# Kernel tuning notes

Hardware: AMD Instinct MI355X
Metric: run time of the kernel (lower is better)

Reference implementation:

```python
import jax, jax.numpy as jnp
import numpy as np

N_PER_GRAPH = 28
E_PER_GRAPH = 56
B = 16384
C = 128
LN_EPS = 1e-5


def setup_inputs() -> dict:
    key = jax.random.key(0)
    k0, k1, k2 = jax.random.split(key, 3)
    N = B * N_PER_GRAPH
    x = jax.random.normal(k0, (N, C), dtype=jnp.float32)
    # graph-local random edges, offset per graph so edge_weights.repeat(B) lines up
    local = jax.random.randint(k1, (2, B * E_PER_GRAPH), 0, N_PER_GRAPH)
    offset = jnp.repeat(jnp.arange(B, dtype=jnp.int64) * N_PER_GRAPH, E_PER_GRAPH)
    edge_index = (local.astype(jnp.int64) + offset[None, :])
    W = jax.random.normal(k2, (C, C), dtype=jnp.float32) * (1.0 / np.sqrt(C))
    bias = jnp.zeros((C,), jnp.float32)
    edge_weights = jnp.ones((E_PER_GRAPH,), jnp.float32)
    gamma = jnp.ones((C,), jnp.float32)
    beta = jnp.zeros((C,), jnp.float32)
    return {"x": x, "edge_index": edge_index, "W": W, "bias": bias,
            "edge_weights": edge_weights, "gamma": gamma, "beta": beta}


def _gcn_conv(x, edge_index, edge_weight, W, bias):
    # PyG GCNConv: linear -> add self loops (w=1) -> sym-normalize -> scatter-add -> +bias
    N = x.shape[0]
    src, dst = edge_index[0], edge_index[1]
    loop = jnp.arange(N, dtype=edge_index.dtype)
    src_f = jnp.concatenate([src, loop])
    dst_f = jnp.concatenate([dst, loop])
    ew_f = jnp.concatenate([edge_weight, jnp.ones((N,), x.dtype)])
    deg = jax.ops.segment_sum(ew_f, dst_f, num_segments=N)
    dinv = jnp.where(deg > 0, jax.lax.rsqrt(deg), 0.0)
    norm = dinv[src_f] * ew_f * dinv[dst_f]          # [E+N]
    h = x @ W                                        # [N, C]
    msg = h[src_f] * norm[:, None]                   # gather + scale
    agg = jax.ops.segment_sum(msg, dst_f, num_segments=N)  # scatter-add
    return agg + bias


def reference(x, edge_index, W, bias, edge_weights, gamma, beta):
    res = x  # in_channels == out_channels -> residual is Identity
    batch_size = x.shape[0] // N_PER_GRAPH
    edge_weight = jnp.tile(edge_weights, batch_size)  # == edge_weights.repeat(B)
    h = _gcn_conv(x, edge_index, edge_weight, W, bias)
    y = h + res
    mu = jnp.mean(y, axis=-1, keepdims=True)
    var = jnp.mean(jnp.square(y - mu), axis=-1, keepdims=True)
    ln = (y - mu) * jax.lax.rsqrt(var + LN_EPS) * gamma + beta
    return jax.nn.relu(ln)
```

## Files before the change

kernel.cpp:

```cpp
#include <hip/hip_runtime.h>

#define NPG 28
#define EPG 56
#define ROWS 56
#define EDG 112
#define CH 128
#define LDW 136

typedef float f32x4 __attribute__((ext_vector_type(4)));
typedef __bf16 bf16x8 __attribute__((ext_vector_type(8)));
typedef unsigned short u16;
typedef u16 u16x8 __attribute__((ext_vector_type(8)));
typedef u16 u16x4 __attribute__((ext_vector_type(4)));

__device__ __forceinline__ u16 f2bf(float f){
  union { float f; unsigned u; } v; v.f = f;
  unsigned r = (v.u + 0x7fffu + ((v.u >> 16) & 1u)) >> 16;
  return (u16)r;
}
__device__ __forceinline__ float bf2f(u16 h){
  union { unsigned u; float f; } v; v.u = ((unsigned)h) << 16;
  return v.f;
}

__global__ __launch_bounds__(256, 2)
void gcn_fused(const float* __restrict__ x, const int* __restrict__ ei,
               const float* __restrict__ W, const float* __restrict__ bias,
               const float* __restrict__ ew, const float* __restrict__ gamma,
               const float* __restrict__ beta, float* __restrict__ out,
               int npairs)
{
  __shared__ alignas(16) u16 Wt[CH][LDW];
  __shared__ alignas(16) u16 Hs[ROWS][LDW];
  __shared__ alignas(16) float gam[CH], bet[CH], bia[CH];
  __shared__ float evw[EPG];
  __shared__ float deg[ROWS];
  __shared__ int   cnt[ROWS];
  __shared__ int   rs[ROWS + 1];
  __shared__ int   c_src[EDG];
  __shared__ float c_nrm[EDG];

  const int tid  = threadIdx.x;
  const int lane = tid & 63;
  const int wv   = tid >> 6;
  const int Etot = npairs * EDG;

  for (int i = tid; i < CH * CH; i += 256){
    Wt[i & (CH - 1)][i >> 7] = f2bf(W[i]);
  }
  if (tid < EPG) evw[tid] = ew[tid];
  if (tid < CH){ gam[tid] = gamma[tid]; bet[tid] = beta[tid]; bia[tid] = bias[tid]; }

  for (int p = blockIdx.x; p < npairs; p += gridDim.x){
    __syncthreads();

    int es = 0, ed = 0; float eww = 0.f;
    if (tid < ROWS) deg[tid] = 1.0f;
    if (tid < EDG){
      es  = ei[p * EDG + tid]        - p * ROWS;
      ed  = ei[Etot + p * EDG + tid] - p * ROWS;
      eww = evw[(tid >= EPG) ? (tid - EPG) : tid];
    }

    int arow = 16 * wv + (lane & 15);
    int grow = p * ROWS + (arow < ROWS ? arow : ROWS - 1);
    const float* xp = x + (size_t)grow * CH + ((lane >> 4) * 8);
    bf16x8 afr[4];
#pragma unroll
    for (int ks = 0; ks < 4; ks++){
      f32x4 lo = *(const f32x4*)(xp + ks * 32);
      f32x4 hi = *(const f32x4*)(xp + ks * 32 + 4);
      u16x8 t;
      t[0] = f2bf(lo[0]); t[1] = f2bf(lo[1]); t[2] = f2bf(lo[2]); t[3] = f2bf(lo[3]);
      t[4] = f2bf(hi[0]); t[5] = f2bf(hi[1]); t[6] = f2bf(hi[2]); t[7] = f2bf(hi[3]);
      afr[ks] = __builtin_bit_cast(bf16x8, t);
    }
    f32x4 acc[8];
#pragma unroll
    for (int ct = 0; ct < 8; ct++){
      acc[ct] = (f32x4){0.f, 0.f, 0.f, 0.f};
      const u16* wp = &Wt[16 * ct + (lane & 15)][(lane >> 4) * 8];
#pragma unroll
      for (int ks = 0; ks < 4; ks++){
        u16x8 b = *(const u16x8*)(wp + ks * 32);
        acc[ct] = __builtin_amdgcn_mfma_f32_16x16x32_bf16(
                    afr[ks], __builtin_bit_cast(bf16x8, b), acc[ct], 0, 0, 0);
      }
    }
    {
      int r0 = 16 * wv + ((lane >> 4) << 2);
      int cc = lane & 15;
#pragma unroll
      for (int ct = 0; ct < 8; ct++){
#pragma unroll
        for (int r = 0; r < 4; r++){
          int rr = r0 + r;
          if (rr < ROWS) Hs[rr][16 * ct + cc] = f2bf(acc[ct][r]);
        }
      }
    }
    __syncthreads();

    if (tid < EDG) atomicAdd(&deg[ed], eww);
    __syncthreads();
    if (tid < ROWS){ deg[tid] = rsqrtf(deg[tid]); cnt[tid] = 0; }
    __syncthreads();
    float nrm = 0.f;
    if (tid < EDG){
      nrm = deg[es] * eww * deg[ed];
      atomicAdd(&cnt[ed], 1);
    }
    __syncthreads();
    if (wv == 0){
      int v = (lane < ROWS) ? cnt[lane] : 0;
#pragma unroll
      for (int off = 1; off < 64; off <<= 1){
        int n = __shfl_up(v, off, 64);
        if (lane >= off) v += n;
      }
      if (lane < ROWS){ rs[lane + 1] = v; cnt[lane] = 0; }
      if (lane == 0) rs[0] = 0;
    }
    __syncthreads();
    if (tid < EDG){
      int slot = rs[ed] + atomicAdd(&cnt[ed], 1);
      c_src[slot] = es;
      c_nrm[slot] = nrm;
    }
    __syncthreads();

    int half = lane >> 5;
    int l32  = lane & 31;
    int c0   = l32 * 4;
    for (int rp = wv; rp < ROWS / 2; rp += 4){
      int row = 2 * rp + half;
      float dv = deg[row];
      float d2 = dv * dv;
      size_t gbase = (size_t)(p * ROWS + row) * CH + c0;
      u16x4 hs = *(const u16x4*)&Hs[row][c0];
      f32x4 xr = *(const f32x4*)(x + gbase);
      f32x4 bb = *(const f32x4*)&bia[c0];
      float y0 = bf2f(hs[0]) * d2 + bb[0] + xr[0];
      float y1 = bf2f(hs[1]) * d2 + bb[1] + xr[1];
      float y2 = bf2f(hs[2]) * d2 + bb[2] + xr[2];
      float y3 = bf2f(hs[3]) * d2 + bb[3] + xr[3];
      int s0 = rs[row], s1 = rs[row + 1];
      for (int i = s0; i < s1; i++){
        int sc = c_src[i]; float nm = c_nrm[i];
        u16x4 hv = *(const u16x4*)&Hs[sc][c0];
        y0 += nm * bf2f(hv[0]);
        y1 += nm * bf2f(hv[1]);
        y2 += nm * bf2f(hv[2]);
        y3 += nm * bf2f(hv[3]);
      }
      float sm = y0 + y1 + y2 + y3;
      float sq = y0*y0 + y1*y1 + y2*y2 + y3*y3;
#pragma unroll
      for (int m = 1; m < 32; m <<= 1){
        sm += __shfl_xor(sm, m, 32);
        sq += __shfl_xor(sq, m, 32);
      }
      float mu   = sm * (1.0f / 128.0f);
      float var  = sq * (1.0f / 128.0f) - mu * mu;
      float rstd = rsqrtf(var + 1e-5f);
      f32x4 g4 = *(const f32x4*)&gam[c0];
      f32x4 b4 = *(const f32x4*)&bet[c0];
      f32x4 o;
      o[0] = fmaxf(0.f, (y0 - mu) * rstd * g4[0] + b4[0]);
      o[1] = fmaxf(0.f, (y1 - mu) * rstd * g4[1] + b4[1]);
      o[2] = fmaxf(0.f, (y2 - mu) * rstd * g4[2] + b4[2]);
      o[3] = fmaxf(0.f, (y3 - mu) * rstd * g4[3] + b4[3]);
      *(f32x4*)(out + gbase) = o;
    }
  }
}

extern "C" void kernel_launch(void* const* d_in, const int* in_sizes, int n_in,
                              void* d_out, int out_size, void* d_ws, size_t ws_size,
                              hipStream_t stream)
{
  const float* x     = (const float*)d_in[0];
  const int*   ei    = (const int*)d_in[1];
  const float* W     = (const float*)d_in[2];
  const float* bias  = (const float*)d_in[3];
  const float* ew    = (const float*)d_in[4];
  const float* gamma = (const float*)d_in[5];
  const float* beta  = (const float*)d_in[6];
  float* out = (float*)d_out;

  int N = in_sizes[0] / CH;
  int npairs = N / ROWS;
  int grid = npairs < 2048 ? npairs : 2048;
  hipLaunchKernelGGL(gcn_fused, dim3(grid), dim3(256), 0, stream,
                     x, ei, W, bias, ew, gamma, beta, out, npairs);
}
```

Before: 159.7 us.

## Process two graph pairs per 512-thread block with x prefetch and prepacked W

A separate pre-kernel packs W into bf16 in MFMA fragment order inside the workspace, so each block does a straight vectorized copy into LDS instead of a strided transpose-and-convert. Each block now runs 512 threads that handle two 56-row pairs at once, with LDS buffers doubled, and it prefetches the next iteration's x rows into registers while the current one finishes. Degree and count atomics are merged into a single pass using a second counter array, which removes several barriers. The costs are more registers and LDS per block, which may limit occupancy, an extra kernel launch, and the assumption that npairs is even.

```diff
diff --git a/kernel.cpp b/kernel.cpp
--- a/kernel.cpp
+++ b/kernel.cpp
@@ -23,53 +23,87 @@
   return v.f;
 }
 
-__global__ __launch_bounds__(256, 2)
+__global__ void pack_w(const float* __restrict__ W, u16* __restrict__ wp){
+  int d = blockIdx.x * 256 + threadIdx.x;
+  int j  = d & 7;
+  int l  = (d >> 3) & 63;
+  int ks = (d >> 9) & 3;
+  int ct = d >> 11;
+  int k = ((l >> 4) << 3) + (ks << 5) + j;
+  int c = (ct << 4) + (l & 15);
+  wp[d] = f2bf(W[k * CH + c]);
+}
+
+__global__ __launch_bounds__(512, 4)
 void gcn_fused(const float* __restrict__ x, const int* __restrict__ ei,
                const float* __restrict__ W, const float* __restrict__ bias,
                const float* __restrict__ ew, const float* __restrict__ gamma,
                const float* __restrict__ beta, float* __restrict__ out,
-               int npairs)
+               const u16* __restrict__ wpack, int npairs)
 {
-  __shared__ alignas(16) u16 Wt[CH][LDW];
-  __shared__ alignas(16) u16 Hs[ROWS][LDW];
-  __shared__ alignas(16) float gam[CH], bet[CH], bia[CH];
-  __shared__ float evw[EPG];
-  __shared__ float deg[ROWS];
-  __shared__ int   cnt[ROWS];
-  __shared__ int   rs[ROWS + 1];
-  __shared__ int   c_src[EDG];
-  __shared__ float c_nrm[EDG];
+  __shared__ alignas(16) u16 Bp[16384];
+  __shared__ alignas(16) u16 Hs[2][ROWS][LDW];
+  __shared__ float gam[CH], bet[CH], bia[CH], evw[EPG];
+  __shared__ float deg[2][ROWS];
+  __shared__ int   cnt[2][ROWS], cnt2[2][ROWS], rs[2][ROWS + 1];
+  __shared__ int   c_src[2][EDG];
+  __shared__ float c_nrm[2][EDG];
 
   const int tid  = threadIdx.x;
   const int lane = tid & 63;
-  const int wv   = tid >> 6;
+  const int s    = tid >> 8;
+  const int wv4  = (tid >> 6) & 3;
+  const int t256 = tid & 255;
+  const int ngroups = npairs >> 1;
   const int Etot = npairs * EDG;
 
-  for (int i = tid; i < CH * CH; i += 256){
-    Wt[i & (CH - 1)][i >> 7] = f2bf(W[i]);
+  if (wpack){
+    for (int it = 0; it < 4; ++it){
+      int idx = it * 512 + tid;
+      *(u16x8*)&Bp[idx * 8] = ((const u16x8*)wpack)[idx];
+    }
+  } else {
+    for (int i = tid; i < CH * CH; i += 512){
+      int j = i & 7, l = (i >> 3) & 63, ks = (i >> 9) & 3, ct = i >> 11;
+      int k = ((l >> 4) << 3) + (ks << 5) + j;
+      int c = (ct << 4) + (l & 15);
+      Bp[i] = f2bf(W[k * CH + c]);
+    }
   }
   if (tid < EPG) evw[tid] = ew[tid];
   if (tid < CH){ gam[tid] = gamma[tid]; bet[tid] = beta[tid]; bia[tid] = bias[tid]; }
 
-  for (int p = blockIdx.x; p < npairs; p += gridDim.x){
+  const int arow = 16 * wv4 + (lane & 15);
+  const int rowc = arow < ROWS ? arow : ROWS - 1;
+  const int xoff = (lane >> 4) * 8;
+
+  f32x4 pf[8];
+  {
+    int p0 = 2 * blockIdx.x + s;
+    const float* xp = x + ((size_t)p0 * ROWS + rowc) * CH + xoff;
+#pragma unroll
+    for (int ks = 0; ks < 4; ks++){
+      pf[2 * ks]     = *(const f32x4*)(xp + ks * 32);
+      pf[2 * ks + 1] = *(const f32x4*)(xp + ks * 32 + 4);
+    }
+  }
+
+  for (int q = blockIdx.x; q < ngroups; q += gridDim.x){
+    const int p = 2 * q + s;
     __syncthreads();
 
     int es = 0, ed = 0; float eww = 0.f;
-    if (tid < ROWS) deg[tid] = 1.0f;
-    if (tid < EDG){
-      es  = ei[p * EDG + tid]        - p * ROWS;
-      ed  = ei[Etot + p * EDG + tid] - p * ROWS;
-      eww = evw[(tid >= EPG) ? (tid - EPG) : tid];
-    }
-
-    int arow = 16 * wv + (lane & 15);
-    int grow = p * ROWS + (arow < ROWS ? arow : ROWS - 1);
-    const float* xp = x + (size_t)grow * CH + ((lane >> 4) * 8);
+    if (t256 < EDG){
+      es  = ei[p * EDG + t256]        - p * ROWS;
+      ed  = ei[Etot + p * EDG + t256] - p * ROWS;
+      eww = evw[(t256 >= EPG) ? (t256 - EPG) : t256];
+    }
+    if (t256 < ROWS){ deg[s][t256] = 1.0f; cnt[s][t256] = 0; cnt2[s][t256] = 0; }
+
     bf16x8 afr[4];
 #pragma unroll
     for (int ks = 0; ks < 4; ks++){
-      f32x4 lo = *(const f32x4*)(xp + ks * 32);
-      f32x4 hi = *(const f32x4*)(xp + ks * 32 + 4);
+      f32x4 lo = pf[2 * ks], hi = pf[2 * ks + 1];
       u16x8 t;
       t[0] = f2bf(lo[0]); t[1] = f2bf(lo[1]); t[2] = f2bf(lo[2]); t[3] = f2bf(lo[3]);
       t[4] = f2bf(hi[0]); t[5] = f2bf(hi[1]); t[6] = f2bf(hi[2]); t[7] = f2bf(hi[3]);
@@ -79,75 +113,83 @@
 #pragma unroll
     for (int ct = 0; ct < 8; ct++){
       acc[ct] = (f32x4){0.f, 0.f, 0.f, 0.f};
-      const u16* wp = &Wt[16 * ct + (lane & 15)][(lane >> 4) * 8];
 #pragma unroll
       for (int ks = 0; ks < 4; ks++){
-        u16x8 b = *(const u16x8*)(wp + ks * 32);
+        u16x8 b = *(const u16x8*)&Bp[(((ct << 2) + ks) * 64 + lane) * 8];
         acc[ct] = __builtin_amdgcn_mfma_f32_16x16x32_bf16(
                     afr[ks], __builtin_bit_cast(bf16x8, b), acc[ct], 0, 0, 0);
       }
     }
     {
-      int r0 = 16 * wv + ((lane >> 4) << 2);
+      int r0 = 16 * wv4 + ((lane >> 4) << 2);
       int cc = lane & 15;
 #pragma unroll
       for (int ct = 0; ct < 8; ct++){
 #pragma unroll
         for (int r = 0; r < 4; r++){
           int rr = r0 + r;
-          if (rr < ROWS) Hs[rr][16 * ct + cc] = f2bf(acc[ct][r]);
+          if (rr < ROWS) Hs[s][rr][16 * ct + cc] = f2bf(acc[ct][r]);
         }
       }
     }
-    __syncthreads();
-
-    if (tid < EDG) atomicAdd(&deg[ed], eww);
-    __syncthreads();
-    if (tid < ROWS){ deg[tid] = rsqrtf(deg[tid]); cnt[tid] = 0; }
-    __syncthreads();
-    float nrm = 0.f;
-    if (tid < EDG){
-      nrm = deg[es] * eww * deg[ed];
-      atomicAdd(&cnt[ed], 1);
-    }
-    __syncthreads();
-    if (wv == 0){
-      int v = (lane < ROWS) ? cnt[lane] : 0;
+    {
+      int qn = q + (int)gridDim.x; if (qn >= ngroups) qn = q;
+      int pn = 2 * qn + s;
+      const float* xp = x + ((size_t)pn * ROWS + rowc) * CH + xoff;
+#pragma unroll
+      for (int ks = 0; ks < 4; ks++){
+        pf[2 * ks]     = *(const f32x4*)(xp + ks * 32);
+        pf[2 * ks + 1] = *(const f32x4*)(xp + ks * 32 + 4);
+      }
+    }
+    __syncthreads();
+
+    if (t256 < EDG){
+      atomicAdd(&deg[s][ed], eww);
+      atomicAdd(&cnt[s][ed], 1);
+    }
+    __syncthreads();
+
+    if (t256 < ROWS) deg[s][t256] = rsqrtf(deg[s][t256]);
+    if (wv4 == 0){
+      int v = (lane < ROWS) ? cnt[s][lane] : 0;
 #pragma unroll
       for (int off = 1; off < 64; off <<= 1){
         int n = __shfl_up(v, off, 64);
         if (lane >= off) v += n;
       }
-      if (lane < ROWS){ rs[lane + 1] = v; cnt[lane] = 0; }
-      if (lane == 0) rs[0] = 0;
-    }
-    __syncthreads();
-    if (tid < EDG){
-      int slot = rs[ed] + atomicAdd(&cnt[ed], 1);
-      c_src[slot] = es;
-      c_nrm[slot] = nrm;
+      if (lane < ROWS) rs[s][lane + 1] = v;
+      if (lane == 0)   rs[s][0] = 0;
+    }
+    __syncthreads();
+
+    if (t256 < EDG){
+      float nrm = deg[s][es] * eww * deg[s][ed];
+      int slot = rs[s][ed] + atomicAdd(&cnt2[s][ed], 1);
+      c_src[s][slot] = es;
+      c_nrm[s][slot] = nrm;
     }
     __syncthreads();
 
     int half = lane >> 5;
     int l32  = lane & 31;
     int c0   = l32 * 4;
-    for (int rp = wv; rp < ROWS / 2; rp += 4){
+    for (int rp = wv4; rp < ROWS / 2; rp += 4){
       int row = 2 * rp + half;
-      float dv = deg[row];
+      float dv = deg[s][row];
       float d2 = dv * dv;
-      size_t gbase = (size_t)(p * ROWS + row) * CH + c0;
-      u16x4 hs = *(const u16x4*)&Hs[row][c0];
+      size_t gbase = ((size_t)p * ROWS + row) * CH + c0;
+      u16x4 hs = *(const u16x4*)&Hs[s][row][c0];
       f32x4 xr = *(const f32x4*)(x + gbase);
       f32x4 bb = *(const f32x4*)&bia[c0];
       float y0 = bf2f(hs[0]) * d2 + bb[0] + xr[0];
       float y1 = bf2f(hs[1]) * d2 + bb[1] + xr[1];
       float y2 = bf2f(hs[2]) * d2 + bb[2] + xr[2];
       float y3 = bf2f(hs[3]) * d2 + bb[3] + xr[3];
-      int s0 = rs[row], s1 = rs[row + 1];
+      int s0 = rs[s][row], s1 = rs[s][row + 1];
       for (int i = s0; i < s1; i++){
-        int sc = c_src[i]; float nm = c_nrm[i];
-        u16x4 hv = *(const u16x4*)&Hs[sc][c0];
+        int sc = c_src[s][i]; float nm = c_nrm[s][i];
+        u16x4 hv = *(const u16x4*)&Hs[s][sc][c0];
         y0 += nm * bf2f(hv[0]);
         y1 += nm * bf2f(hv[1]);
         y2 += nm * bf2f(hv[2]);
@@ -190,7 +232,15 @@
 
   int N = in_sizes[0] / CH;
   int npairs = N / ROWS;
-  int grid = npairs < 2048 ? npairs : 2048;
-  hipLaunchKernelGGL(gcn_fused, dim3(grid), dim3(256), 0, stream,
-                     x, ei, W, bias, ew, gamma, beta, out, npairs);
-}
+  int ngroups = npairs / 2;
+
+  u16* wpack = nullptr;
+  if (ws_size >= (size_t)(CH * CH * sizeof(u16))){
+    wpack = (u16*)d_ws;
+    hipLaunchKernelGGL(pack_w, dim3(CH * CH / 256), dim3(256), 0, stream, W, wpack);
+  }
+
+  int grid = ngroups < 1024 ? ngroups : 1024;
+  hipLaunchKernelGGL(gcn_fused, dim3(grid), dim3(512), 0, stream,
+                     x, ei, W, bias, ew, gamma, beta, out, wpack, npairs);
+}
```

Measured after the change: 138.0 us. 1.16x faster.

## Prepack W in a separate kernel and launch one block per graph pair

Applied to the files above, without the earlier changes.

A small pre-kernel converts W to bf16 once, in MFMA fragment order, into the workspace. The main kernel now reads its B fragments straight from global memory (L2-resident) instead of having every persistent block transpose W into shared memory. The persistent loop is replaced by one block per 56-row tile, with launch bounds raised to 8 blocks per SM, and the row-count and degree passes are merged to cut barriers. The residual is taken from the bf16 x registers rather than re-read from global, which adds rounding error, and the epilogue now works on MFMA-row ownership with 8-wide vectors.

```diff
diff --git a/kernel.cpp b/kernel.cpp
--- a/kernel.cpp
+++ b/kernel.cpp
@@ -11,7 +11,6 @@
 typedef __bf16 bf16x8 __attribute__((ext_vector_type(8)));
 typedef unsigned short u16;
 typedef u16 u16x8 __attribute__((ext_vector_type(8)));
-typedef u16 u16x4 __attribute__((ext_vector_type(4)));
 
 __device__ __forceinline__ u16 f2bf(float f){
   union { float f; unsigned u; } v; v.f = f;
@@ -23,154 +22,178 @@
   return v.f;
 }
 
-__global__ __launch_bounds__(256, 2)
+__global__ void pack_w(const float* __restrict__ W, u16* __restrict__ wp){
+  int d = blockIdx.x * 256 + threadIdx.x;
+  int j  = d & 7;
+  int l  = (d >> 3) & 63;
+  int ks = (d >> 9) & 3;
+  int ct = d >> 11;
+  int k = ((l >> 4) << 3) + (ks << 5) + j;
+  int c = (ct << 4) + (l & 15);
+  wp[d] = f2bf(W[k * CH + c]);
+}
+
+__global__ __launch_bounds__(256, 8)
 void gcn_fused(const float* __restrict__ x, const int* __restrict__ ei,
                const float* __restrict__ W, const float* __restrict__ bias,
                const float* __restrict__ ew, const float* __restrict__ gamma,
                const float* __restrict__ beta, float* __restrict__ out,
-               int npairs)
+               const u16* __restrict__ wpack, int npairs)
 {
-  __shared__ alignas(16) u16 Wt[CH][LDW];
   __shared__ alignas(16) u16 Hs[ROWS][LDW];
-  __shared__ alignas(16) float gam[CH], bet[CH], bia[CH];
-  __shared__ float evw[EPG];
+  __shared__ float gbb[3][CH];
   __shared__ float deg[ROWS];
-  __shared__ int   cnt[ROWS];
-  __shared__ int   rs[ROWS + 1];
+  __shared__ int   cnt[ROWS], cnt2[ROWS], rs[ROWS + 1];
   __shared__ int   c_src[EDG];
   __shared__ float c_nrm[EDG];
 
   const int tid  = threadIdx.x;
   const int lane = tid & 63;
   const int wv   = tid >> 6;
+  const int hi   = lane >> 4;
+  const int p    = blockIdx.x;
   const int Etot = npairs * EDG;
 
-  for (int i = tid; i < CH * CH; i += 256){
-    Wt[i & (CH - 1)][i >> 7] = f2bf(W[i]);
-  }
-  if (tid < EPG) evw[tid] = ew[tid];
-  if (tid < CH){ gam[tid] = gamma[tid]; bet[tid] = beta[tid]; bia[tid] = bias[tid]; }
-
-  for (int p = blockIdx.x; p < npairs; p += gridDim.x){
-    __syncthreads();
-
-    int es = 0, ed = 0; float eww = 0.f;
-    if (tid < ROWS) deg[tid] = 1.0f;
-    if (tid < EDG){
-      es  = ei[p * EDG + tid]        - p * ROWS;
-      ed  = ei[Etot + p * EDG + tid] - p * ROWS;
-      eww = evw[(tid >= EPG) ? (tid - EPG) : tid];
-    }
-
-    int arow = 16 * wv + (lane & 15);
-    int grow = p * ROWS + (arow < ROWS ? arow : ROWS - 1);
-    const float* xp = x + (size_t)grow * CH + ((lane >> 4) * 8);
-    bf16x8 afr[4];
+  int es = 0, ed = 0; float eww = 0.f;
+  if (tid < EDG){
+    es  = ei[p * EDG + tid]        - p * ROWS;
+    ed  = ei[Etot + p * EDG + tid] - p * ROWS;
+    eww = ew[(tid >= EPG) ? (tid - EPG) : tid];
+  }
+  if (tid < ROWS){ deg[tid] = 1.0f; cnt[tid] = 0; cnt2[tid] = 0; }
+  if (tid < CH){
+    gbb[0][tid] = gamma[tid]; gbb[1][tid] = beta[tid]; gbb[2][tid] = bias[tid];
+  }
+
+  const int arow = 16 * wv + (lane & 15);
+  const int rowc = arow < ROWS ? arow : ROWS - 1;
+  const float* xp = x + ((size_t)p * ROWS + rowc) * CH + hi * 8;
+  bf16x8 afr[4];
+#pragma unroll
+  for (int ks = 0; ks < 4; ks++){
+    f32x4 lo = *(const f32x4*)(xp + ks * 32);
+    f32x4 h4 = *(const f32x4*)(xp + ks * 32 + 4);
+    u16x8 t;
+    t[0] = f2bf(lo[0]); t[1] = f2bf(lo[1]); t[2] = f2bf(lo[2]); t[3] = f2bf(lo[3]);
+    t[4] = f2bf(h4[0]); t[5] = f2bf(h4[1]); t[6] = f2bf(h4[2]); t[7] = f2bf(h4[3]);
+    afr[ks] = __builtin_bit_cast(bf16x8, t);
+  }
+
+  f32x4 acc[8];
+#pragma unroll
+  for (int ct = 0; ct < 8; ct++){
+    acc[ct] = (f32x4){0.f, 0.f, 0.f, 0.f};
 #pragma unroll
     for (int ks = 0; ks < 4; ks++){
-      f32x4 lo = *(const f32x4*)(xp + ks * 32);
-      f32x4 hi = *(const f32x4*)(xp + ks * 32 + 4);
-      u16x8 t;
-      t[0] = f2bf(lo[0]); t[1] = f2bf(lo[1]); t[2] = f2bf(lo[2]); t[3] = f2bf(lo[3]);
-      t[4] = f2bf(hi[0]); t[5] = f2bf(hi[1]); t[6] = f2bf(hi[2]); t[7] = f2bf(hi[3]);
-      afr[ks] = __builtin_bit_cast(bf16x8, t);
-    }
-    f32x4 acc[8];
+      u16x8 b;
+      if (wpack){
+        b = ((const u16x8*)wpack)[((ct << 2) + ks) * 64 + lane];
+      } else {
+#pragma unroll
+        for (int j = 0; j < 8; j++){
+          int k = hi * 8 + ks * 32 + j;
+          int c = ct * 16 + (lane & 15);
+          b[j] = f2bf(W[k * CH + c]);
+        }
+      }
+      acc[ct] = __builtin_amdgcn_mfma_f32_16x16x32_bf16(
+                  afr[ks], __builtin_bit_cast(bf16x8, b), acc[ct], 0, 0, 0);
+    }
+  }
+  {
+    int r0 = 16 * wv + (hi << 2);
+    int cc = lane & 15;
 #pragma unroll
     for (int ct = 0; ct < 8; ct++){
-      acc[ct] = (f32x4){0.f, 0.f, 0.f, 0.f};
-      const u16* wp = &Wt[16 * ct + (lane & 15)][(lane >> 4) * 8];
+#pragma unroll
+      for (int r = 0; r < 4; r++){
+        int rr = r0 + r;
+        if (rr < ROWS) Hs[rr][16 * ct + cc] = f2bf(acc[ct][r]);
+      }
+    }
+  }
+  __syncthreads();
+
+  if (tid < EDG){
+    atomicAdd(&deg[ed], eww);
+    atomicAdd(&cnt[ed], 1);
+  }
+  __syncthreads();
+
+  if (tid < ROWS) deg[tid] = rsqrtf(deg[tid]);
+  if (wv == 0){
+    int v = (lane < ROWS) ? cnt[lane] : 0;
+#pragma unroll
+    for (int off = 1; off < 64; off <<= 1){
+      int n = __shfl_up(v, off, 64);
+      if (lane >= off) v += n;
+    }
+    if (lane < ROWS) rs[lane + 1] = v;
+    if (lane == 0)   rs[0] = 0;
+  }
+  __syncthreads();
+
+  if (tid < EDG){
+    float nrm = deg[es] * eww * deg[ed];
+    int slot = rs[ed] + atomicAdd(&cnt2[ed], 1);
+    c_src[slot] = es;
+    c_nrm[slot] = nrm;
+  }
+  __syncthreads();
+
+  if (arow < ROWS){
+    const int row = arow;
+    const int cb  = hi * 8;
+    float dv = deg[row];
+    float d2 = dv * dv;
+    float y[4][8];
+#pragma unroll
+    for (int ks = 0; ks < 4; ks++){
+      u16x8 hv = *(const u16x8*)&Hs[row][cb + ks * 32];
+      u16x8 xr = __builtin_bit_cast(u16x8, afr[ks]);
+      f32x4 b0 = *(const f32x4*)&gbb[2][cb + ks * 32];
+      f32x4 b1 = *(const f32x4*)&gbb[2][cb + ks * 32 + 4];
+#pragma unroll
+      for (int j = 0; j < 8; j++){
+        float bb = j < 4 ? b0[j] : b1[j - 4];
+        y[ks][j] = bf2f(hv[j]) * d2 + bb + bf2f(xr[j]);
+      }
+    }
+    int s0 = rs[row], s1 = rs[row + 1];
+    for (int i = s0; i < s1; i++){
+      int sc = c_src[i]; float nm = c_nrm[i];
 #pragma unroll
       for (int ks = 0; ks < 4; ks++){
-        u16x8 b = *(const u16x8*)(wp + ks * 32);
-        acc[ct] = __builtin_amdgcn_mfma_f32_16x16x32_bf16(
-                    afr[ks], __builtin_bit_cast(bf16x8, b), acc[ct], 0, 0, 0);
-      }
-    }
-    {
-      int r0 = 16 * wv + ((lane >> 4) << 2);
-      int cc = lane & 15;
-#pragma unroll
-      for (int ct = 0; ct < 8; ct++){
-#pragma unroll
-        for (int r = 0; r < 4; r++){
-          int rr = r0 + r;
-          if (rr < ROWS) Hs[rr][16 * ct + cc] = f2bf(acc[ct][r]);
-        }
-      }
-    }
-    __syncthreads();
-
-    if (tid < EDG) atomicAdd(&deg[ed], eww);
-    __syncthreads();
-    if (tid < ROWS){ deg[tid] = rsqrtf(deg[tid]); cnt[tid] = 0; }
-    __syncthreads();
-    float nrm = 0.f;
-    if (tid < EDG){
-      nrm = deg[es] * eww * deg[ed];
-      atomicAdd(&cnt[ed], 1);
-    }
-    __syncthreads();
-    if (wv == 0){
-      int v = (lane < ROWS) ? cnt[lane] : 0;
-#pragma unroll
-      for (int off = 1; off < 64; off <<= 1){
-        int n = __shfl_up(v, off, 64);
-        if (lane >= off) v += n;
-      }
-      if (lane < ROWS){ rs[lane + 1] = v; cnt[lane] = 0; }
-      if (lane == 0) rs[0] = 0;
-    }
-    __syncthreads();
-    if (tid < EDG){
-      int slot = rs[ed] + atomicAdd(&cnt[ed], 1);
-      c_src[slot] = es;
-      c_nrm[slot] = nrm;
-    }
-    __syncthreads();
-
-    int half = lane >> 5;
-    int l32  = lane & 31;
-    int c0   = l32 * 4;
-    for (int rp = wv; rp < ROWS / 2; rp += 4){
-      int row = 2 * rp + half;
-      float dv = deg[row];
-      float d2 = dv * dv;
-      size_t gbase = (size_t)(p * ROWS + row) * CH + c0;
-      u16x4 hs = *(const u16x4*)&Hs[row][c0];
-      f32x4 xr = *(const f32x4*)(x + gbase);
-      f32x4 bb = *(const f32x4*)&bia[c0];
-      float y0 = bf2f(hs[0]) * d2 + bb[0] + xr[0];
-      float y1 = bf2f(hs[1]) * d2 + bb[1] + xr[1];
-      float y2 = bf2f(hs[2]) * d2 + bb[2] + xr[2];
-      float y3 = bf2f(hs[3]) * d2 + bb[3] + xr[3];
-      int s0 = rs[row], s1 = rs[row + 1];
-      for (int i = s0; i < s1; i++){
-        int sc = c_src[i]; float nm = c_nrm[i];
-        u16x4 hv = *(const u16x4*)&Hs[sc][c0];
-        y0 += nm * bf2f(hv[0]);
-        y1 += nm * bf2f(hv[1]);
-        y2 += nm * bf2f(hv[2]);
-        y3 += nm * bf2f(hv[3]);
-      }
-      float sm = y0 + y1 + y2 + y3;
-      float sq = y0*y0 + y1*y1 + y2*y2 + y3*y3;
-#pragma unroll
-      for (int m = 1; m < 32; m <<= 1){
-        sm += __shfl_xor(sm, m, 32);
-        sq += __shfl_xor(sq, m, 32);
-      }
-      float mu   = sm * (1.0f / 128.0f);
-      float var  = sq * (1.0f / 128.0f) - mu * mu;
-      float rstd = rsqrtf(var + 1e-5f);
-      f32x4 g4 = *(const f32x4*)&gam[c0];
-      f32x4 b4 = *(const f32x4*)&bet[c0];
-      f32x4 o;
-      o[0] = fmaxf(0.f, (y0 - mu) * rstd * g4[0] + b4[0]);
-      o[1] = fmaxf(0.f, (y1 - mu) * rstd * g4[1] + b4[1]);
-      o[2] = fmaxf(0.f, (y2 - mu) * rstd * g4[2] + b4[2]);
-      o[3] = fmaxf(0.f, (y3 - mu) * rstd * g4[3] + b4[3]);
-      *(f32x4*)(out + gbase) = o;
+        u16x8 hv = *(const u16x8*)&Hs[sc][cb + ks * 32];
+#pragma unroll
+        for (int j = 0; j < 8; j++) y[ks][j] += nm * bf2f(hv[j]);
+      }
+    }
+    float sm = 0.f, sq = 0.f;
+#pragma unroll
+    for (int ks = 0; ks < 4; ks++)
+#pragma unroll
+      for (int j = 0; j < 8; j++){ sm += y[ks][j]; sq += y[ks][j] * y[ks][j]; }
+    sm += __shfl_xor(sm, 16); sq += __shfl_xor(sq, 16);
+    sm += __shfl_xor(sm, 32); sq += __shfl_xor(sq, 32);
+    float mu   = sm * (1.0f / 128.0f);
+    float var  = sq * (1.0f / 128.0f) - mu * mu;
+    float rstd = rsqrtf(var + 1e-5f);
+    size_t gbase = ((size_t)p * ROWS + row) * CH + cb;
+#pragma unroll
+    for (int ks = 0; ks < 4; ks++){
+      f32x4 g0 = *(const f32x4*)&gbb[0][cb + ks * 32];
+      f32x4 g1 = *(const f32x4*)&gbb[0][cb + ks * 32 + 4];
+      f32x4 t0 = *(const f32x4*)&gbb[1][cb + ks * 32];
+      f32x4 t1 = *(const f32x4*)&gbb[1][cb + ks * 32 + 4];
+      f32x4 o0, o1;
+#pragma unroll
+      for (int j = 0; j < 4; j++){
+        o0[j] = fmaxf(0.f, (y[ks][j]     - mu) * rstd * g0[j] + t0[j]);
+        o1[j] = fmaxf(0.f, (y[ks][j + 4] - mu) * rstd * g1[j] + t1[j]);
+      }
+      *(f32x4*)(out + gbase + ks * 32)     = o0;
+      *(f32x4*)(out + gbase + ks * 32 + 4) = o1;
     }
   }
 }
@@ -190,7 +213,13 @@
 
   int N = in_sizes[0] / CH;
   int npairs = N / ROWS;
-  int grid = npairs < 2048 ? npairs : 2048;
-  hipLaunchKernelGGL(gcn_fused, dim3(grid), dim3(256), 0, stream,
-                     x, ei, W, bias, ew, gamma, beta, out, npairs);
-}
+
+  u16* wpack = nullptr;
+  if (ws_size >= (size_t)(CH * CH * sizeof(u16))){
+    wpack = (u16*)d_ws;
+    hipLaunchKernelGGL(pack_w, dim3(CH * CH / 256), dim3(256), 0, stream, W, wpack);
+  }
+
+  hipLaunchKernelGGL(gcn_fused, dim3(npairs), dim3(256), 0, stream,
+                     x, ei, W, bias, ew, gamma, beta, out, wpack, npairs);
+}
```

After: 225.3 us. 41.1% more time.
